# Kernel optimization log

Hardware: AMD Instinct MI355X
Metric: run time of the kernel (lower is better)

The kernel has to match this reference:

```python
import jax, jax.numpy as jnp
import numpy as np

NUM_EXPERTS = 16  # init_kwargs


def setup_inputs() -> dict:
    key = jax.random.key(0)
    k1, k2, k3 = jax.random.split(key, 3)
    T, D = 8192, 1024
    inp = jax.random.normal(k1, (T, D), dtype=jnp.float32)
    domain_ids = jax.random.randint(k2, (T,), 0, NUM_EXPERTS, dtype=jnp.int32)
    mask = jax.random.bernoulli(k3, 0.1, (T,))
    return {"input": inp, "domain_ids": domain_ids, "mask": mask}


def reference(input, domain_ids, mask):
    T = input.shape[0]
    E = NUM_EXPERTS
    capacity = -(-T // E)  # math.ceil(num_tokens / num_experts)

    # one_hot(domain_ids, num_experts) -> [T, E] (integer, as in torch util)
    mask1 = jax.nn.one_hot(domain_ids, E, dtype=jnp.int32)
    # zero out padded tokens: mask1 * (~mask)
    mask1 = mask1 * (~mask)[:, None].astype(jnp.int32)

    # fused_cumsum_sub_one: cumsum over token dim minus 1 -> position within expert
    locations1 = jnp.cumsum(mask1, axis=0) - 1  # [T, E]

    # drop tokens beyond expert capacity
    mask1 = mask1 * (locations1 < capacity).astype(jnp.int32)

    # capacity slot index for each token (0 where dropped)
    locations1_s = jnp.sum(locations1 * mask1, axis=1)  # [T]

    # gates1_s = ones -> gates1 = mask1 as float
    gates1 = mask1.astype(input.dtype)  # [T, E]

    # one_hot over capacity slots, [T, C]
    loc_sc = jax.nn.one_hot(locations1_s, capacity, dtype=input.dtype)

    # bmm([T,E,1], [T,1,C]) == batched outer product -> [T, E, C]
    combine1_sec = gates1[:, :, None] * loc_sc[:, None, :]
    dispatch_mask = combine1_sec.astype(bool)

    l_aux = jnp.zeros((), dtype=input.dtype)
    return (l_aux, combine1_sec, dispatch_mask)
```

## Files before the change

kernel.cpp:

```cpp
#include <hip/hip_runtime.h>
#include <hip/hip_bf16.h>


#define T_TOKENS 8192
#define NUM_EXPERTS 16
#define CAPACITY 512
#define TEC ((size_t)T_TOKENS * NUM_EXPERTS * CAPACITY)

__global__ __launch_bounds__(1024)
void DomainGate_68908455297139_kernel(const int* __restrict__ domain_ids,
                                      const void* __restrict__ mask_raw,
                                      float* __restrict__ out) {
    __shared__ int s_packed;
    if (threadIdx.x == 0) s_packed = 0;
    __syncthreads();

    const int* mw = (const int*)mask_raw;
    int bad = 0;
    for (int i = threadIdx.x; i < 2048; i += 1024) {
        if ((unsigned)mw[i] > 1u) bad = 1;
    }
    if (bad) s_packed = 1;
    __syncthreads();
    const bool packed = (s_packed != 0);
    const unsigned char* mb = (const unsigned char*)mask_raw;

    const int wave = threadIdx.x >> 6;
    const int lane = threadIdx.x & 63;

    int running = 0;
    const unsigned long long lane_lt = (lane == 0) ? 0ull : ((1ull << lane) - 1ull);

    for (int c = 0; c < T_TOKENS / 64; ++c) {
        const int t = c * 64 + lane;
        const int e = domain_ids[t];
        const bool is_pad = packed ? (mb[t] != 0) : (mw[t] != 0);
        const bool match = (e == wave) && !is_pad;
        const unsigned long long b = __ballot(match);
        if (match) {
            const int pos = running + __popcll(b & lane_lt);
            if (pos < CAPACITY) {
                const size_t idx = 1ull + ((size_t)t * NUM_EXPERTS + wave) * CAPACITY + (size_t)pos;
                out[idx] = 1.0f;
                out[idx + TEC] = 1.0f;
            }
        }
        running += __popcll(b);
    }
}

extern "C" void kernel_launch(void* const* d_in, const int* in_sizes, int n_in,
                              void* d_out, int out_size, void* d_ws, size_t ws_size,
                              hipStream_t stream) {
    (void)in_sizes; (void)n_in; (void)d_ws; (void)ws_size;
    const int* domain_ids = (const int*)d_in[1];
    const void* mask_raw = d_in[2];
    float* out = (float*)d_out;

    hipMemsetAsync(out, 0, (size_t)out_size * sizeof(float), stream);

    DomainGate_68908455297139_kernel<<<1, 1024, 0, stream>>>(domain_ids, mask_raw, out);
}
```

Measured before the change: 595.6 us.

## Replace memset plus scatter with prep kernel and dense fused fill kernel

Splits the work into a single-block prep kernel that computes each token's capacity slot per expert into a workspace array, and a grid-stride fill kernel that writes the entire output with float4 stores, emitting ones where the column matches the slot. This removes the separate full-buffer memset and the scattered single-float writes, so the output is written once densely. The prep kernel also processes four tokens per lane with vectorized loads to shorten the serial scan. The cost is an extra workspace read per output element and an unaligned-offset computation per element in the fill.

```diff
diff --git a/kernel.cpp b/kernel.cpp
--- a/kernel.cpp
+++ b/kernel.cpp
@@ -5,21 +5,21 @@
 #define T_TOKENS 8192
 #define NUM_EXPERTS 16
 #define CAPACITY 512
-#define TEC ((size_t)T_TOKENS * NUM_EXPERTS * CAPACITY)
+#define TEC (67108864ull)
+#define TOTAL (134217729ull)
 
 __global__ __launch_bounds__(1024)
-void DomainGate_68908455297139_kernel(const int* __restrict__ domain_ids,
-                                      const void* __restrict__ mask_raw,
-                                      float* __restrict__ out) {
+void DomainGate_prep(const int* __restrict__ domain_ids,
+                     const void* __restrict__ mask_raw,
+                     int* __restrict__ rowinfo ) {
     __shared__ int s_packed;
     if (threadIdx.x == 0) s_packed = 0;
     __syncthreads();
 
     const int* mw = (const int*)mask_raw;
     int bad = 0;
-    for (int i = threadIdx.x; i < 2048; i += 1024) {
+    for (int i = threadIdx.x; i < 2048; i += 1024)
         if ((unsigned)mw[i] > 1u) bad = 1;
-    }
     if (bad) s_packed = 1;
     __syncthreads();
     const bool packed = (s_packed != 0);
@@ -27,37 +27,89 @@
 
     const int wave = threadIdx.x >> 6;
     const int lane = threadIdx.x & 63;
+    const unsigned long long lane_lt = (lane == 0) ? 0ull : ((1ull << lane) - 1ull);
 
     int running = 0;
-    const unsigned long long lane_lt = (lane == 0) ? 0ull : ((1ull << lane) - 1ull);
+    for (int c = 0; c < T_TOKENS / 256; ++c) {
+        const int t0 = c * 256 + lane * 4;
+        const int4 e4 = *(const int4*)&domain_ids[t0];
 
-    for (int c = 0; c < T_TOKENS / 64; ++c) {
-        const int t = c * 64 + lane;
-        const int e = domain_ids[t];
-        const bool is_pad = packed ? (mb[t] != 0) : (mw[t] != 0);
-        const bool match = (e == wave) && !is_pad;
-        const unsigned long long b = __ballot(match);
-        if (match) {
-            const int pos = running + __popcll(b & lane_lt);
-            if (pos < CAPACITY) {
-                const size_t idx = 1ull + ((size_t)t * NUM_EXPERTS + wave) * CAPACITY + (size_t)pos;
-                out[idx] = 1.0f;
-                out[idx + TEC] = 1.0f;
+        int p0, p1, p2, p3;
+        if (packed) {
+            p0 = mb[t0 + 0]; p1 = mb[t0 + 1]; p2 = mb[t0 + 2]; p3 = mb[t0 + 3];
+        } else {
+            const int4 m4 = *(const int4*)&mw[t0];
+            p0 = m4.x; p1 = m4.y; p2 = m4.z; p3 = m4.w;
+        }
+        const int b0 = (e4.x == wave) && !p0;
+        const int b1 = (e4.y == wave) && !p1;
+        const int b2 = (e4.z == wave) && !p2;
+        const int b3 = (e4.w == wave) && !p3;
+
+        const unsigned long long B0 = __ballot(b0);
+        const unsigned long long B1 = __ballot(b1);
+        const unsigned long long B2 = __ballot(b2);
+        const unsigned long long B3 = __ballot(b3);
+
+        const int before = __popcll(B0 & lane_lt) + __popcll(B1 & lane_lt) +
+                           __popcll(B2 & lane_lt) + __popcll(B3 & lane_lt);
+        const int r0 = running + before;
+        const int r1 = r0 + b0;
+        const int r2 = r1 + b1;
+        const int r3 = r2 + b2;
+
+        int4 o;
+        o.x = (b0 && r0 < CAPACITY) ? r0 : -1;
+        o.y = (b1 && r1 < CAPACITY) ? r1 : -1;
+        o.z = (b2 && r2 < CAPACITY) ? r2 : -1;
+        o.w = (b3 && r3 < CAPACITY) ? r3 : -1;
+        *(int4*)&rowinfo[wave * T_TOKENS + t0] = o;
+
+        running += __popcll(B0) + __popcll(B1) + __popcll(B2) + __popcll(B3);
+    }
+}
+
+__global__ __launch_bounds__(256)
+void DomainGate_fill(const int* __restrict__ rowinfo, float* __restrict__ out) {
+    const size_t ngroups = TOTAL >> 2;
+    const size_t stride = (size_t)gridDim.x * blockDim.x;
+    size_t g = (size_t)blockIdx.x * blockDim.x + threadIdx.x;
+
+    if (g == 0) {
+        const size_t r = TOTAL - 2 - TEC;
+        const int row = (int)(r >> 9), c = (int)(r & 511);
+        const int op = rowinfo[((row & 15) << 13) | (row >> 4)];
+        out[TOTAL - 1] = (c == op) ? 1.0f : 0.0f;
+    }
+
+    for (; g < ngroups; g += stride) {
+        float vals[4];
+        #pragma unroll
+        for (int j = 0; j < 4; ++j) {
+            const size_t f = 4 * g + (size_t)j;
+            float v = 0.0f;
+            if (f != 0) {
+                size_t r = f - 1;
+                if (r >= TEC) r -= TEC;
+                const int row = (int)(r >> 9), c = (int)(r & 511);
+                const int op = rowinfo[((row & 15) << 13) | (row >> 4)];
+                v = (c == op) ? 1.0f : 0.0f;
             }
+            vals[j] = v;
         }
-        running += __popcll(b);
+        *(float4*)&out[4 * g] = make_float4(vals[0], vals[1], vals[2], vals[3]);
     }
 }
 
 extern "C" void kernel_launch(void* const* d_in, const int* in_sizes, int n_in,
                               void* d_out, int out_size, void* d_ws, size_t ws_size,
                               hipStream_t stream) {
-    (void)in_sizes; (void)n_in; (void)d_ws; (void)ws_size;
+    (void)in_sizes; (void)n_in; (void)out_size; (void)ws_size;
     const int* domain_ids = (const int*)d_in[1];
     const void* mask_raw = d_in[2];
     float* out = (float*)d_out;
+    int* rowinfo = (int*)d_ws;
 
-    hipMemsetAsync(out, 0, (size_t)out_size * sizeof(float), stream);
-
-    DomainGate_68908455297139_kernel<<<1, 1024, 0, stream>>>(domain_ids, mask_raw, out);
+    DomainGate_prep<<<1, 1024, 0, stream>>>(domain_ids, mask_raw, rowinfo);
+    DomainGate_fill<<<2048, 256, 0, stream>>>(rowinfo, out);
 }
```

Result: faster. 567.0 us (-4.8%).
